# Kernel optimization log

Hardware: AMD Instinct MI355X
Metric: run time of the kernel (lower is better)

The kernel has to match this reference:

```python
import jax, jax.numpy as jnp
import numpy as np

B, N, L = 16, 512, 512          # batch, compound atoms, protein words
DIM = 10                         # compound feature dim
DM, H, DK, DFF = 128, 8, 16, 512 # transformer dims
LG, LO = 3, 3                    # layer_gnn, layer_output
NFP, NW = 10000, 10000           # vocab sizes
NEG = -9e15                      # GAT mask sentinel (matches torch code)


def _layernorm(x, g, b, eps=1e-6):
    # annotated-transformer LayerNorm: unbiased std, eps added to std
    m = jnp.mean(x, -1, keepdims=True)
    s = jnp.std(x, -1, keepdims=True, ddof=1)
    return g * (x - m) / (s + eps) + b


def _pos_encoding(length, d_model):
    pos = np.arange(length)[:, None]
    div = np.exp(np.arange(0, d_model, 2) * (-np.log(10000.0) / d_model))
    pe = np.zeros((length, d_model), np.float32)
    pe[:, 0::2] = np.sin(pos * div)
    pe[:, 1::2] = np.cos(pos * div)
    return jnp.asarray(pe)


def setup_inputs():
    ks = iter(jax.random.split(jax.random.key(0), 64))
    def nrm(shape, scale):
        return jax.random.normal(next(ks), shape, jnp.float32) * scale
    return dict(
        fingerprints=jax.random.randint(next(ks), (B, N), 0, NFP, jnp.int32),
        fp_mask=jnp.ones((B, N), jnp.float32),
        adjacency=jax.random.randint(next(ks), (B, N, N), 0, 2, jnp.int32),
        words=jax.random.randint(next(ks), (B, L), 0, NW, jnp.int32),
        words_mask=jnp.ones((B, L), jnp.float32),
        emb_fp=nrm((NFP, DIM), 0.1),
        emb_word=nrm((NW, DM), 0.1),
        Wg=nrm((LG, DIM, DIM), 0.3), bg=jnp.zeros((LG, DIM), jnp.float32),
        attn_a=nrm((LG, 2 * DIM), 0.3),
        Wq=nrm((DM, DM), 0.09), bq=jnp.zeros((DM,), jnp.float32),
        Wk=nrm((DM, DM), 0.09), bk=jnp.zeros((DM,), jnp.float32),
        Wv=nrm((DM, DM), 0.09), bv=jnp.zeros((DM,), jnp.float32),
        Wo=nrm((DM, DM), 0.09), bo=jnp.zeros((DM,), jnp.float32),
        ln1_g=jnp.ones((DM,), jnp.float32), ln1_b=jnp.zeros((DM,), jnp.float32),
        ln2_g=jnp.ones((DM,), jnp.float32), ln2_b=jnp.zeros((DM,), jnp.float32),
        lnf_g=jnp.ones((DM,), jnp.float32), lnf_b=jnp.zeros((DM,), jnp.float32),
        W1=nrm((DM, DFF), 0.09), b1=jnp.zeros((DFF,), jnp.float32),
        W2=nrm((DFF, DM), 0.045), b2=jnp.zeros((DM,), jnp.float32),
        Wtout=nrm((DM, DIM), 0.09), btout=jnp.zeros((DIM,), jnp.float32),
        Watt=nrm((DIM, DIM), 0.3), batt=jnp.zeros((DIM,), jnp.float32),
        Wout=nrm((LO, 2 * DIM, 2 * DIM), 0.2), bout=jnp.zeros((LO, 2 * DIM), jnp.float32),
        Wint=nrm((2 * DIM, 2), 0.2), bint=jnp.zeros((2,), jnp.float32),
    )


def _forward(fingerprints, fp_mask, adjacency, words, words_mask,
             emb_fp, emb_word, Wg, bg, attn_a,
             Wq, bq, Wk, bk, Wv, bv, Wo, bo,
             ln1_g, ln1_b, ln2_g, ln2_b, lnf_g, lnf_b,
             W1, b1, W2, b2, Wtout, btout,
             Watt, batt, Wout, bout, Wint, bint):
    # ---- GAT over compound graph (dropout disabled = eval/deterministic) ----
    xs = emb_fp[fingerprints]                     # [B,N,DIM]
    mask = fp_mask[:, :, None]                    # [B,N,1]
    adj = adjacency > 0
    for i in range(LG):
        h = jax.nn.relu(xs @ Wg[i] + bg[i]) * mask
        # e[b,i,j] = leaky_relu(a1.h_i + a2.h_j)  == leaky_relu([h_i||h_j] @ a)
        s1 = h @ attn_a[i, :DIM]                  # [B,N]
        s2 = h @ attn_a[i, DIM:]                  # [B,N]
        e = jax.nn.leaky_relu(s1[:, :, None] + s2[:, None, :])  # [B,N,N]
        att = jax.nn.softmax(jnp.where(adj, e, NEG), axis=2)
        xs = xs + att @ h
    compound = jnp.mean(xs * mask, axis=1, keepdims=True)       # [B,1,DIM]

    # ---- transformer encoder, 1 layer, annotated-transformer (pre-norm) ----
    x = emb_word[words] * jnp.sqrt(jnp.float32(DM)) + _pos_encoding(L, DM)
    m4 = words_mask[:, None, None, :] > 0         # [B,1,1,L]
    xn = _layernorm(x, ln1_g, ln1_b)
    heads = lambda t: t.reshape(B, L, H, DK).transpose(0, 2, 1, 3)
    q, k, v = heads(xn @ Wq + bq), heads(xn @ Wk + bk), heads(xn @ Wv + bv)
    scores = jnp.einsum('bhqd,bhkd->bhqk', q, k) / jnp.sqrt(jnp.float32(DK))
    p = jax.nn.softmax(jnp.where(m4, scores, -1e9), axis=-1)
    attn = jnp.einsum('bhqk,bhkd->bhqd', p, v).transpose(0, 2, 1, 3).reshape(B, L, DM)
    x = x + (attn @ Wo + bo)
    xn = _layernorm(x, ln2_g, ln2_b)
    x = x + (jax.nn.relu(xn @ W1 + b1) @ W2 + b2)
    x = _layernorm(x, lnf_g, lnf_b)
    word_vectors = jax.nn.relu(x) @ Wtout + btout  # [B,L,DIM]

    # ---- tanh cross-attention (attention_cnn) ----
    hc = jax.nn.relu(compound @ Watt + batt)       # [B,1,DIM]
    hp = jax.nn.relu(word_vectors @ Watt + batt)   # [B,L,DIM]
    w = jnp.tanh(jnp.einsum('bxd,bld->bxl', hc, hp))  # [B,1,L]
    protein = jnp.mean(w.transpose(0, 2, 1) * hp, axis=1, keepdims=True)  # [B,1,DIM]

    cat = jnp.concatenate([compound, protein], axis=2)  # [B,1,2*DIM]
    for j in range(LO):
        cat = jax.nn.relu(cat @ Wout[j] + bout[j])
    return jnp.squeeze(cat @ Wint + bint, axis=1)        # [B,2]


def reference(fingerprints, fp_mask, adjacency, words, words_mask,
              emb_fp, emb_word, Wg, bg, attn_a,
              Wq, bq, Wk, bk, Wv, bv, Wo, bo,
              ln1_g, ln1_b, ln2_g, ln2_b, lnf_g, lnf_b,
              W1, b1, W2, b2, Wtout, btout,
              Watt, batt, Wout, bout, Wint, bint):
    return _forward(fingerprints, fp_mask, adjacency, words, words_mask,
                    emb_fp, emb_word, Wg, bg, attn_a,
                    Wq, bq, Wk, bk, Wv, bv, Wo, bo,
                    ln1_g, ln1_b, ln2_g, ln2_b, lnf_g, lnf_b,
                    W1, b1, W2, b2, Wtout, btout,
                    Watt, batt, Wout, bout, Wint, bint)
```

## Files before the change

### kernel.cpp

```cpp
#include <hip/hip_runtime.h>
#include <hip/hip_bf16.h>
#include <math.h>

#define B 16
#define N 512
#define L 512
#define DIM 10
#define DM 128
#define H 8
#define DK 16
#define DFF 512
#define LG 3
#define LO 3
#define NEGV -9.0e15f
#define RF 16
#define AQR 64

__device__ __forceinline__ float wave_reduce_sum(float v) {
    #pragma unroll
    for (int o = 32; o > 0; o >>= 1) v += __shfl_down(v, o, 64);
    return v;
}


__global__ void k_embed_fp(const int* __restrict__ fing, const float* __restrict__ emb_fp,
                           float* __restrict__ xs) {
    int idx = blockIdx.x * blockDim.x + threadIdx.x;
    if (idx >= B * N * DIM) return;
    int d = idx % DIM;
    int bn = idx / DIM;
    xs[idx] = emb_fp[fing[bn] * DIM + d];
}

__global__ void k_gnn_h(const float* __restrict__ xs, const float* __restrict__ fp_mask,
                        const float* __restrict__ Wg, const float* __restrict__ bg,
                        const float* __restrict__ aatt,
                        float* __restrict__ h, float* __restrict__ s1, float* __restrict__ s2) {
    int bn = blockIdx.x * blockDim.x + threadIdx.x;
    if (bn >= B * N) return;
    float x[DIM];
    #pragma unroll
    for (int d = 0; d < DIM; d++) x[d] = xs[bn * DIM + d];
    float m = fp_mask[bn];
    float a1 = 0.f, a2 = 0.f;
    #pragma unroll
    for (int j = 0; j < DIM; j++) {
        float acc = bg[j];
        #pragma unroll
        for (int d = 0; d < DIM; d++) acc += x[d] * Wg[d * DIM + j];
        acc = fmaxf(acc, 0.f) * m;
        h[bn * DIM + j] = acc;
        a1 += acc * aatt[j];
        a2 += acc * aatt[DIM + j];
    }
    s1[bn] = a1;
    s2[bn] = a2;
}

__global__ void k_gnn_att(const float* __restrict__ h, const float* __restrict__ s1,
                          const float* __restrict__ s2, const int* __restrict__ adj,
                          float* __restrict__ xs) {
    int b  = blockIdx.x / (N / 16);
    int rg = blockIdx.x % (N / 16);
    int t = threadIdx.x;
    int g  = t >> 4;
    int ll = t & 15;
    int i = rg * 16 + g;

    __shared__ float h_s[N * DIM];
    __shared__ float s2_s[N];

    const float* hb = h + (long)b * N * DIM;
    for (int idx = t; idx < N * DIM; idx += 256) h_s[idx] = hb[idx];
    for (int j = t; j < N; j += 256) s2_s[j] = s2[b * N + j];
    __syncthreads();

    float s1v = s1[b * N + i];
    const int* adjrow = adj + ((long)b * N + i) * N;

    float e[32];
    #pragma unroll
    for (int c = 0; c < 32; c++) {
        int j = c * 16 + ll;
        float xsc = s1v + s2_s[j];
        xsc = xsc > 0.f ? xsc : 0.01f * xsc;
        e[c] = (adjrow[j] > 0) ? xsc : NEGV;
    }
    float m = e[0];
    #pragma unroll
    for (int c = 1; c < 32; c++) m = fmaxf(m, e[c]);
    #pragma unroll
    for (int off = 1; off < 16; off <<= 1) m = fmaxf(m, __shfl_xor(m, off, 64));

    float sum = 0.f;
    float a[DIM];
    #pragma unroll
    for (int d = 0; d < DIM; d++) a[d] = 0.f;
    #pragma unroll
    for (int c = 0; c < 32; c++) {
        float p = expf(e[c] - m);
        sum += p;
        int j = c * 16 + ll;
        #pragma unroll
        for (int d = 0; d < DIM; d++) a[d] += p * h_s[j * DIM + d];
    }
    #pragma unroll
    for (int off = 1; off < 16; off <<= 1) {
        sum += __shfl_xor(sum, off, 64);
        #pragma unroll
        for (int d = 0; d < DIM; d++) a[d] += __shfl_xor(a[d], off, 64);
    }
    if (ll < DIM) {
        float av = a[0];
        if (ll == 1) av = a[1]; else if (ll == 2) av = a[2]; else if (ll == 3) av = a[3];
        else if (ll == 4) av = a[4]; else if (ll == 5) av = a[5]; else if (ll == 6) av = a[6];
        else if (ll == 7) av = a[7]; else if (ll == 8) av = a[8]; else if (ll == 9) av = a[9];
        xs[((long)b * N + i) * DIM + ll] += av / sum;
    }
}

__global__ void k_compound(const float* __restrict__ xs, const float* __restrict__ fp_mask,
                           const float* __restrict__ Watt, const float* __restrict__ batt,
                           float* __restrict__ compound, float* __restrict__ hc) {
    int b = blockIdx.x;
    int t = threadIdx.x;
    int wid = t >> 6, lane = t & 63;
    float lacc[DIM];
    #pragma unroll
    for (int d = 0; d < DIM; d++) lacc[d] = 0.f;
    for (int n = t; n < N; n += 256) {
        float m = fp_mask[b * N + n];
        #pragma unroll
        for (int d = 0; d < DIM; d++) lacc[d] += xs[((long)b * N + n) * DIM + d] * m;
    }
    __shared__ float red[4][DIM];
    __shared__ float comp_s[DIM];
    #pragma unroll
    for (int d = 0; d < DIM; d++) lacc[d] = wave_reduce_sum(lacc[d]);
    if (lane == 0) {
        #pragma unroll
        for (int d = 0; d < DIM; d++) red[wid][d] = lacc[d];
    }
    __syncthreads();
    if (t < DIM) {
        float c = (red[0][t] + red[1][t] + red[2][t] + red[3][t]) / (float)N;
        compound[b * DIM + t] = c;
        comp_s[t] = c;
    }
    __syncthreads();
    if (t < DIM) {
        float acc = batt[t];
        #pragma unroll
        for (int e = 0; e < DIM; e++) acc += comp_s[e] * Watt[e * DIM + t];
        hc[b * DIM + t] = fmaxf(acc, 0.f);
    }
}


__global__ void k_pe(float* __restrict__ pe) {
    int idx = blockIdx.x * blockDim.x + threadIdx.x;
    if (idx >= L * DM) return;
    int d = idx % DM, l = idx / DM;
    int k = d >> 1;
    double div = exp((double)(2 * k) * (-log(10000.0) / (double)DM));
    double ang = (double)l * div;
    pe[idx] = (d & 1) ? (float)cos(ang) : (float)sin(ang);
}

__global__ void k_embed_word(const int* __restrict__ words, const float* __restrict__ emb,
                             const float* __restrict__ pe, float* __restrict__ x) {
    long idx = (long)blockIdx.x * blockDim.x + threadIdx.x;
    if (idx >= (long)B * L * DM) return;
    int d = idx % DM;
    long bl = idx / DM;
    int l = (int)(bl % L);
    x[idx] = emb[(long)words[bl] * DM + d] * sqrtf(128.0f) + pe[l * DM + d];
}

__global__ void k_layernorm(const float* __restrict__ x, const float* __restrict__ g,
                            const float* __restrict__ bb, float* __restrict__ out) {
    int row = blockIdx.x;
    int t = threadIdx.x;
    int wid = t >> 6, lane = t & 63;
    float v = x[(long)row * DM + t];
    float s = wave_reduce_sum(v);
    __shared__ float r2[2], r3[2];
    if (lane == 0) r2[wid] = s;
    __syncthreads();
    float mean = (r2[0] + r2[1]) / (float)DM;
    float dv = v - mean;
    float q = wave_reduce_sum(dv * dv);
    if (lane == 0) r3[wid] = q;
    __syncthreads();
    float sd = sqrtf((r3[0] + r3[1]) / (float)(DM - 1)) + 1e-6f;
    out[(long)row * DM + t] = g[t] * dv / sd + bb[t];
}

__global__ void k_qkv(const float* __restrict__ xn,
                      const float* __restrict__ Wq, const float* __restrict__ bq,
                      const float* __restrict__ Wk, const float* __restrict__ bk,
                      const float* __restrict__ Wv, const float* __restrict__ bv,
                      float* __restrict__ q, float* __restrict__ k, float* __restrict__ v) {
    long row0 = (long)blockIdx.x * RF;
    int t = threadIdx.x;
    __shared__ float xs_s[RF * DM];
    for (int i = t; i < RF * DM; i += 384) xs_s[i] = xn[row0 * DM + i];
    __syncthreads();
    int proj = t / DM;
    int j = t % DM;
    const float* W    = proj == 0 ? Wq : (proj == 1 ? Wk : Wv);
    const float* bias = proj == 0 ? bq : (proj == 1 ? bk : bv);
    float* out        = proj == 0 ? q  : (proj == 1 ? k  : v);
    float acc[RF];
    #pragma unroll
    for (int r = 0; r < RF; r++) acc[r] = bias[j];
    for (int d = 0; d < DM; d++) {
        float w = W[d * DM + j];
        #pragma unroll
        for (int r = 0; r < RF; r++) acc[r] += xs_s[r * DM + d] * w;
    }
    #pragma unroll
    for (int r = 0; r < RF; r++) {
        long row = row0 + r;
        int b = (int)(row / L), l = (int)(row % L);
        out[(((long)b * H + j / DK) * L + l) * DK + (j % DK)] = acc[r];
    }
}

__global__ void k_attn(const float* __restrict__ q, const float* __restrict__ k,
                       const float* __restrict__ v, const float* __restrict__ wmask,
                       float* __restrict__ attnout) {
    int blk = blockIdx.x;
    int qc = blk % (L / AQR);
    int bh = blk / (L / AQR);
    int b = bh / H, hh = bh % H;
    int t = threadIdx.x;
    int sl = t & 3;
    int r = t >> 2;
    int l = qc * AQR + r;

    __shared__ float4 k_s[L * 4];
    __shared__ float wm_s[L];
    const float4* kb4 = (const float4*)(k + (long)bh * L * DK);
    for (int i = t; i < L * 4; i += 256) k_s[i] = kb4[i];
    for (int j = t; j < L; j += 256) wm_s[j] = wmask[b * L + j];
    __syncthreads();

    float4 qr = ((const float4*)(q + ((long)bh * L + l) * DK))[sl];
    qr.x *= 0.25f; qr.y *= 0.25f; qr.z *= 0.25f; qr.w *= 0.25f;

    const float4* vb4 = (const float4*)(v + (long)bh * L * DK);

    float m = -1e30f, ssum = 0.f;
    float4 acc = make_float4(0.f, 0.f, 0.f, 0.f);

    for (int c = 0; c < L / 8; c++) {
        int j0 = c * 8;
        float s8[8];
        #pragma unroll
        for (int jj = 0; jj < 8; jj++) {
            float4 kk = k_s[(j0 + jj) * 4 + sl];
            s8[jj] = qr.x * kk.x + qr.y * kk.y + qr.z * kk.z + qr.w * kk.w;
        }
        #pragma unroll
        for (int jj = 0; jj < 8; jj++) {
            s8[jj] += __shfl_xor(s8[jj], 1, 64);
            s8[jj] += __shfl_xor(s8[jj], 2, 64);
            s8[jj] = (wm_s[j0 + jj] > 0.f) ? s8[jj] : -1e9f;
        }
        float cm = fmaxf(fmaxf(fmaxf(s8[0], s8[1]), fmaxf(s8[2], s8[3])),
                         fmaxf(fmaxf(s8[4], s8[5]), fmaxf(s8[6], s8[7])));
        float mn = fmaxf(m, cm);
        float scale = __expf(m - mn);
        ssum *= scale;
        acc.x *= scale; acc.y *= scale; acc.z *= scale; acc.w *= scale;
        #pragma unroll
        for (int jj = 0; jj < 8; jj++) {
            float p = __expf(s8[jj] - mn);
            ssum += p;
            float4 vv = vb4[(j0 + jj) * 4 + sl];
            acc.x += p * vv.x; acc.y += p * vv.y; acc.z += p * vv.z; acc.w += p * vv.w;
        }
        m = mn;
    }

    float inv = 1.f / ssum;
    float4* outp = (float4*)(attnout + ((long)b * L + l) * DM + hh * DK);
    outp[sl] = make_float4(acc.x * inv, acc.y * inv, acc.z * inv, acc.w * inv);
}

__global__ void k_oproj(const float* __restrict__ attnout, const float* __restrict__ Wo,
                        const float* __restrict__ bo, float* __restrict__ x) {
    long row0 = (long)blockIdx.x * RF;
    int t = threadIdx.x;
    __shared__ float a_s[RF * DM];
    for (int i = t; i < RF * DM; i += 128) a_s[i] = attnout[row0 * DM + i];
    __syncthreads();
    float acc[RF];
    #pragma unroll
    for (int r = 0; r < RF; r++) acc[r] = bo[t];
    for (int d = 0; d < DM; d++) {
        float w = Wo[d * DM + t];
        #pragma unroll
        for (int r = 0; r < RF; r++) acc[r] += a_s[r * DM + d] * w;
    }
    #pragma unroll
    for (int r = 0; r < RF; r++) x[(row0 + r) * DM + t] += acc[r];
}

__global__ void k_ffn(const float* __restrict__ xn, const float* __restrict__ W1,
                      const float* __restrict__ b1, const float* __restrict__ W2,
                      const float* __restrict__ b2, float* __restrict__ x) {
    long row0 = (long)blockIdx.x * RF;
    int t = threadIdx.x;
    __shared__ float xs_s[RF * DM];
    __shared__ float h_s[RF * DFF];
    for (int i = t; i < RF * DM; i += 512) xs_s[i] = xn[row0 * DM + i];
    __syncthreads();
    {
        float acc[RF];
        #pragma unroll
        for (int r = 0; r < RF; r++) acc[r] = b1[t];
        for (int d = 0; d < DM; d++) {
            float w = W1[d * DFF + t];
            #pragma unroll
            for (int r = 0; r < RF; r++) acc[r] += xs_s[r * DM + d] * w;
        }
        #pragma unroll
        for (int r = 0; r < RF; r++) h_s[r * DFF + t] = fmaxf(acc[r], 0.f);
    }
    __syncthreads();
    int col = t & 127, rq = t >> 7;
    float acc2[4];
    #pragma unroll
    for (int rr = 0; rr < 4; rr++) acc2[rr] = b2[col];
    for (int f = 0; f < DFF; f++) {
        float w = W2[f * DM + col];
        #pragma unroll
        for (int rr = 0; rr < 4; rr++) acc2[rr] += h_s[(rq * 4 + rr) * DFF + f] * w;
    }
    #pragma unroll
    for (int rr = 0; rr < 4; rr++) x[(row0 + rq * 4 + rr) * DM + col] += acc2[rr];
}

__global__ void k_lnf_hp(const float* __restrict__ x, const float* __restrict__ g,
                         const float* __restrict__ bb, const float* __restrict__ Wtout,
                         const float* __restrict__ btout, const float* __restrict__ Watt,
                         const float* __restrict__ batt, float* __restrict__ hp) {
    int row = blockIdx.x;
    int t = threadIdx.x;
    int wid = t >> 6, lane = t & 63;
    float v = x[(long)row * DM + t];
    float s = wave_reduce_sum(v);
    __shared__ float r2[2], r3[2];
    if (lane == 0) r2[wid] = s;
    __syncthreads();
    float mean = (r2[0] + r2[1]) / (float)DM;
    float dv = v - mean;
    float qq = wave_reduce_sum(dv * dv);
    if (lane == 0) r3[wid] = qq;
    __syncthreads();
    float sd = sqrtf((r3[0] + r3[1]) / (float)(DM - 1)) + 1e-6f;
    float xnv = g[t] * dv / sd + bb[t];
    __shared__ float rrelu[DM];
    rrelu[t] = fmaxf(xnv, 0.f);
    __syncthreads();
    __shared__ float wv_s[DIM];
    if (t < DIM) {
        float acc = btout[t];
        for (int d = 0; d < DM; d++) acc += rrelu[d] * Wtout[d * DIM + t];
        wv_s[t] = acc;
    }
    __syncthreads();
    if (t < DIM) {
        float acc = batt[t];
        #pragma unroll
        for (int e = 0; e < DIM; e++) acc += wv_s[e] * Watt[e * DIM + t];
        hp[(long)row * DIM + t] = fmaxf(acc, 0.f);
    }
}

__global__ void k_final(const float* __restrict__ hp, const float* __restrict__ hc,
                        const float* __restrict__ compound, const float* __restrict__ Wout,
                        const float* __restrict__ bout, const float* __restrict__ Wint,
                        const float* __restrict__ bint, float* __restrict__ out) {
    int b = blockIdx.x;
    int t = threadIdx.x;
    int wid = t >> 6, lane = t & 63;

    __shared__ float wout_s[LO * 2 * DIM * 2 * DIM];
    __shared__ float bout_s[LO * 2 * DIM];
    __shared__ float wint_s[2 * DIM * 2];
    __shared__ float bint_s[2];
    __shared__ float hc_s[DIM];
    __shared__ float red[4][DIM];
    __shared__ float cat_s[2 * DIM];
    __shared__ float tmp_s[2 * DIM];

    for (int i = t; i < LO * 2 * DIM * 2 * DIM; i += 256) wout_s[i] = Wout[i];
    for (int i = t; i < LO * 2 * DIM; i += 256) bout_s[i] = bout[i];
    for (int i = t; i < 2 * DIM * 2; i += 256) wint_s[i] = Wint[i];
    if (t < 2) bint_s[t] = bint[t];
    if (t < DIM) hc_s[t] = hc[b * DIM + t];
    __syncthreads();

    float lacc[DIM];
    #pragma unroll
    for (int e = 0; e < DIM; e++) lacc[e] = 0.f;
    for (int l = t; l < L; l += 256) {
        const float* hpl = hp + ((long)b * L + l) * DIM;
        float hv[DIM];
        float dot = 0.f;
        #pragma unroll
        for (int e = 0; e < DIM; e++) { hv[e] = hpl[e]; dot += hc_s[e] * hv[e]; }
        float w = tanhf(dot);
        #pragma unroll
        for (int e = 0; e < DIM; e++) lacc[e] += w * hv[e];
    }
    #pragma unroll
    for (int e = 0; e < DIM; e++) lacc[e] = wave_reduce_sum(lacc[e]);
    if (lane == 0) {
        #pragma unroll
        for (int e = 0; e < DIM; e++) red[wid][e] = lacc[e];
    }
    __syncthreads();
    if (t < DIM) {
        cat_s[t] = compound[b * DIM + t];
        cat_s[DIM + t] = (red[0][t] + red[1][t] + red[2][t] + red[3][t]) / (float)L;
    }
    __syncthreads();

    for (int j = 0; j < LO; j++) {
        float acc = 0.f;
        if (t < 2 * DIM) {
            acc = bout_s[j * 2 * DIM + t];
            #pragma unroll
            for (int e = 0; e < 2 * DIM; e++)
                acc += cat_s[e] * wout_s[j * 2 * DIM * 2 * DIM + e * 2 * DIM + t];
            acc = fmaxf(acc, 0.f);
            tmp_s[t] = acc;
        }
        __syncthreads();
        if (t < 2 * DIM) cat_s[t] = tmp_s[t];
        __syncthreads();
    }
    if (t < 2) {
        float o = bint_s[t];
        #pragma unroll
        for (int e = 0; e < 2 * DIM; e++) o += cat_s[e] * wint_s[e * 2 + t];
        out[b * 2 + t] = o;
    }
}

extern "C" void kernel_launch(void* const* d_in, const int* in_sizes, int n_in,
                              void* d_out, int out_size, void* d_ws, size_t ws_size,
                              hipStream_t stream) {
    (void)in_sizes; (void)n_in; (void)out_size; (void)ws_size;
    const int*   fingerprints = (const int*)d_in[0];
    const float* fp_mask      = (const float*)d_in[1];
    const int*   adjacency    = (const int*)d_in[2];
    const int*   words        = (const int*)d_in[3];
    const float* words_mask   = (const float*)d_in[4];
    const float* emb_fp       = (const float*)d_in[5];
    const float* emb_word     = (const float*)d_in[6];
    const float* Wg   = (const float*)d_in[7];
    const float* bg   = (const float*)d_in[8];
    const float* attn_a = (const float*)d_in[9];
    const float* Wq = (const float*)d_in[10];
    const float* bq = (const float*)d_in[11];
    const float* Wk = (const float*)d_in[12];
    const float* bk = (const float*)d_in[13];
    const float* Wv = (const float*)d_in[14];
    const float* bv = (const float*)d_in[15];
    const float* Wo = (const float*)d_in[16];
    const float* bo = (const float*)d_in[17];
    const float* ln1_g = (const float*)d_in[18];
    const float* ln1_b = (const float*)d_in[19];
    const float* ln2_g = (const float*)d_in[20];
    const float* ln2_b = (const float*)d_in[21];
    const float* lnf_g = (const float*)d_in[22];
    const float* lnf_b = (const float*)d_in[23];
    const float* W1 = (const float*)d_in[24];
    const float* b1 = (const float*)d_in[25];
    const float* W2 = (const float*)d_in[26];
    const float* b2 = (const float*)d_in[27];
    const float* Wtout = (const float*)d_in[28];
    const float* btout = (const float*)d_in[29];
    const float* Watt  = (const float*)d_in[30];
    const float* batt  = (const float*)d_in[31];
    const float* Wout  = (const float*)d_in[32];
    const float* bout  = (const float*)d_in[33];
    const float* Wint  = (const float*)d_in[34];
    const float* bint  = (const float*)d_in[35];
    float* out = (float*)d_out;

    float* w = (float*)d_ws;
    float* xs = w;        w += B * N * DIM;
    float* h  = w;        w += B * N * DIM;
    float* s1 = w;        w += B * N;
    float* s2 = w;        w += B * N;
    float* compound = w;  w += B * DIM;
    float* hc = w;        w += B * DIM;
    float* pe = w;        w += L * DM;
    float* x  = w;        w += (long)B * L * DM;
    float* xn = w;        w += (long)B * L * DM;
    float* qb = w;        w += (long)B * H * L * DK;
    float* kb = w;        w += (long)B * H * L * DK;
    float* vb = w;        w += (long)B * H * L * DK;
    float* attnout = w;   w += (long)B * L * DM;
    float* hp = w;        w += (long)B * L * DIM;

    k_embed_fp<<<(B * N * DIM + 255) / 256, 256, 0, stream>>>(fingerprints, emb_fp, xs);
    for (int i = 0; i < LG; i++) {
        k_gnn_h<<<(B * N + 255) / 256, 256, 0, stream>>>(
            xs, fp_mask, Wg + i * DIM * DIM, bg + i * DIM, attn_a + i * 2 * DIM, h, s1, s2);
        k_gnn_att<<<B * (N / 16), 256, 0, stream>>>(h, s1, s2, adjacency, xs);
    }
    k_compound<<<B, 256, 0, stream>>>(xs, fp_mask, Watt, batt, compound, hc);

    k_pe<<<(L * DM + 255) / 256, 256, 0, stream>>>(pe);
    k_embed_word<<<(B * L * DM + 255) / 256, 256, 0, stream>>>(words, emb_word, pe, x);
    k_layernorm<<<B * L, DM, 0, stream>>>(x, ln1_g, ln1_b, xn);
    k_qkv<<<B * L / RF, 3 * DM, 0, stream>>>(xn, Wq, bq, Wk, bk, Wv, bv, qb, kb, vb);
    k_attn<<<B * H * (L / AQR), 256, 0, stream>>>(qb, kb, vb, words_mask, attnout);
    k_oproj<<<B * L / RF, DM, 0, stream>>>(attnout, Wo, bo, x);
    k_layernorm<<<B * L, DM, 0, stream>>>(x, ln2_g, ln2_b, xn);
    k_ffn<<<B * L / RF, DFF, 0, stream>>>(xn, W1, b1, W2, b2, x);
    k_lnf_hp<<<B * L, DM, 0, stream>>>(x, lnf_g, lnf_b, Wtout, btout, Watt, batt, hp);
    k_final<<<B, 256, 0, stream>>>(hp, hc, compound, Wout, bout, Wint, bint, out);
}
```

Before: 277.1 us.

## Restructure attention with split-key threads and double-buffered K/V tiles

Rewrites the attention kernel so each query row is handled by 8 threads that each own a slice of keys, rather than 4 threads splitting the head dimension with shuffle reductions per score. K and V are streamed through double-buffered, swizzled shared-memory tiles of 64 keys, with next-tile global loads issued before compute, and V now comes from LDS instead of global memory. Per-thread online-softmax partials are merged with xor shuffles at the end. The block size doubles to 512 threads with launch bounds of 1, which raises register pressure and adds a barrier per tile.

```diff
diff --git a/kernel.cpp b/kernel.cpp
--- a/kernel.cpp
+++ b/kernel.cpp
@@ -15,11 +15,21 @@
 #define NEGV -9.0e15f
 #define RF 16
 #define AQR 64
+#define KT 64
+#define NT (L / KT)
 
 __device__ __forceinline__ float wave_reduce_sum(float v) {
     #pragma unroll
     for (int o = 32; o > 0; o >>= 1) v += __shfl_down(v, o, 64);
     return v;
+}
+
+__device__ __forceinline__ float dot16(float4 q0, float4 q1, float4 q2, float4 q3,
+                                       float4 k0, float4 k1, float4 k2, float4 k3) {
+    return q0.x*k0.x + q0.y*k0.y + q0.z*k0.z + q0.w*k0.w
+         + q1.x*k1.x + q1.y*k1.y + q1.z*k1.z + q1.w*k1.w
+         + q2.x*k2.x + q2.y*k2.y + q2.z*k2.z + q2.w*k2.w
+         + q3.x*k3.x + q3.y*k3.y + q3.z*k3.z + q3.w*k3.w;
 }
 
 
@@ -227,66 +237,131 @@
     }
 }
 
-__global__ void k_attn(const float* __restrict__ q, const float* __restrict__ k,
-                       const float* __restrict__ v, const float* __restrict__ wmask,
-                       float* __restrict__ attnout) {
+__global__ void __launch_bounds__(512, 1)
+k_attn(const float* __restrict__ q, const float* __restrict__ k,
+       const float* __restrict__ v, const float* __restrict__ wmask,
+       float* __restrict__ attnout) {
     int blk = blockIdx.x;
     int qc = blk % (L / AQR);
     int bh = blk / (L / AQR);
     int b = bh / H, hh = bh % H;
     int t = threadIdx.x;
-    int sl = t & 3;
-    int r = t >> 2;
-    int l = qc * AQR + r;
-
-    __shared__ float4 k_s[L * 4];
-    __shared__ float wm_s[L];
+    int qg = t >> 3;
+    int kg = t & 7;
+    int l = qc * AQR + qg;
+
+    __shared__ float kbuf[2][KT * DK];
+    __shared__ float vbuf[2][KT * DK];
+    __shared__ float madd[2][KT];
+
     const float4* kb4 = (const float4*)(k + (long)bh * L * DK);
-    for (int i = t; i < L * 4; i += 256) k_s[i] = kb4[i];
-    for (int j = t; j < L; j += 256) wm_s[j] = wmask[b * L + j];
-    __syncthreads();
-
-    float4 qr = ((const float4*)(q + ((long)bh * L + l) * DK))[sl];
-    qr.x *= 0.25f; qr.y *= 0.25f; qr.z *= 0.25f; qr.w *= 0.25f;
-
     const float4* vb4 = (const float4*)(v + (long)bh * L * DK);
-
-    float m = -1e30f, ssum = 0.f;
-    float4 acc = make_float4(0.f, 0.f, 0.f, 0.f);
-
-    for (int c = 0; c < L / 8; c++) {
-        int j0 = c * 8;
-        float s8[8];
-        #pragma unroll
-        for (int jj = 0; jj < 8; jj++) {
-            float4 kk = k_s[(j0 + jj) * 4 + sl];
-            s8[jj] = qr.x * kk.x + qr.y * kk.y + qr.z * kk.z + qr.w * kk.w;
+    const float*  wm  = wmask + (long)b * L;
+
+    const float4* qp = (const float4*)(q + ((long)bh * L + l) * DK);
+    float4 q0 = qp[0], q1 = qp[1], q2 = qp[2], q3 = qp[3];
+    q0.x*=0.25f;q0.y*=0.25f;q0.z*=0.25f;q0.w*=0.25f;
+    q1.x*=0.25f;q1.y*=0.25f;q1.z*=0.25f;q1.w*=0.25f;
+    q2.x*=0.25f;q2.y*=0.25f;q2.z*=0.25f;q2.w*=0.25f;
+    q3.x*=0.25f;q3.y*=0.25f;q3.z*=0.25f;q3.w*=0.25f;
+
+    int si = t & 255;
+    int skey = si >> 2, sc = si & 3;
+    int gch = sc ^ ((skey >> 3) & 3);
+    const float4* gsrc = (t < 256) ? kb4 : vb4;
+    long gidx = (long)skey * 4 + gch;
+
+    {
+        float4 r = gsrc[gidx];
+        float* dst = (t < 256) ? &kbuf[0][0] : &vbuf[0][0];
+        ((float4*)dst)[si] = r;
+        if (t < KT) madd[0][t] = (wm[t] > 0.f) ? 0.f : -1e9f;
+    }
+    __syncthreads();
+
+    float m = -1e30f, ss = 0.f;
+    float4 a0 = make_float4(0,0,0,0), a1 = a0, a2 = a0, a3 = a0;
+    int swz = kg & 3;
+
+    int cur = 0;
+    for (int tt = 0; tt < NT; tt++) {
+        float4 pre;
+        float mpre = 1.f;
+        if (tt < NT - 1) {
+            pre = gsrc[(long)(tt + 1) * KT * 4 + gidx];
+            if (t < KT) mpre = wm[(tt + 1) * KT + t];
         }
-        #pragma unroll
-        for (int jj = 0; jj < 8; jj++) {
-            s8[jj] += __shfl_xor(s8[jj], 1, 64);
-            s8[jj] += __shfl_xor(s8[jj], 2, 64);
-            s8[jj] = (wm_s[j0 + jj] > 0.f) ? s8[jj] : -1e9f;
+
+        float s[8];
+        #pragma unroll
+        for (int kk = 0; kk < 8; kk++) {
+            const float4* kp = (const float4*)&kbuf[cur][(kg * 8 + kk) * DK];
+            float4 k0 = kp[0 ^ swz], k1 = kp[1 ^ swz], k2 = kp[2 ^ swz], k3 = kp[3 ^ swz];
+            s[kk] = dot16(q0, q1, q2, q3, k0, k1, k2, k3);
         }
-        float cm = fmaxf(fmaxf(fmaxf(s8[0], s8[1]), fmaxf(s8[2], s8[3])),
-                         fmaxf(fmaxf(s8[4], s8[5]), fmaxf(s8[6], s8[7])));
+        {
+            const float4* mp = (const float4*)&madd[cur][kg * 8];
+            float4 ma = mp[0], mb_ = mp[1];
+            s[0] += ma.x;  s[1] += ma.y;  s[2] += ma.z;  s[3] += ma.w;
+            s[4] += mb_.x; s[5] += mb_.y; s[6] += mb_.z; s[7] += mb_.w;
+        }
+
+        float cm = fmaxf(fmaxf(fmaxf(s[0], s[1]), fmaxf(s[2], s[3])),
+                         fmaxf(fmaxf(s[4], s[5]), fmaxf(s[6], s[7])));
         float mn = fmaxf(m, cm);
         float scale = __expf(m - mn);
-        ssum *= scale;
-        acc.x *= scale; acc.y *= scale; acc.z *= scale; acc.w *= scale;
-        #pragma unroll
-        for (int jj = 0; jj < 8; jj++) {
-            float p = __expf(s8[jj] - mn);
-            ssum += p;
-            float4 vv = vb4[(j0 + jj) * 4 + sl];
-            acc.x += p * vv.x; acc.y += p * vv.y; acc.z += p * vv.z; acc.w += p * vv.w;
+        m = mn;
+        float pls = 0.f;
+        #pragma unroll
+        for (int kk = 0; kk < 8; kk++) { s[kk] = __expf(s[kk] - mn); pls += s[kk]; }
+        ss = ss * scale + pls;
+        a0.x*=scale;a0.y*=scale;a0.z*=scale;a0.w*=scale;
+        a1.x*=scale;a1.y*=scale;a1.z*=scale;a1.w*=scale;
+        a2.x*=scale;a2.y*=scale;a2.z*=scale;a2.w*=scale;
+        a3.x*=scale;a3.y*=scale;a3.z*=scale;a3.w*=scale;
+
+        #pragma unroll
+        for (int kk = 0; kk < 8; kk++) {
+            const float4* vp = (const float4*)&vbuf[cur][(kg * 8 + kk) * DK];
+            float4 v0 = vp[0 ^ swz], v1 = vp[1 ^ swz], v2 = vp[2 ^ swz], v3 = vp[3 ^ swz];
+            float p = s[kk];
+            a0.x += p*v0.x; a0.y += p*v0.y; a0.z += p*v0.z; a0.w += p*v0.w;
+            a1.x += p*v1.x; a1.y += p*v1.y; a1.z += p*v1.z; a1.w += p*v1.w;
+            a2.x += p*v2.x; a2.y += p*v2.y; a2.z += p*v2.z; a2.w += p*v2.w;
+            a3.x += p*v3.x; a3.y += p*v3.y; a3.z += p*v3.z; a3.w += p*v3.w;
         }
+
+        if (tt < NT - 1) {
+            float* dst = (t < 256) ? &kbuf[cur ^ 1][0] : &vbuf[cur ^ 1][0];
+            ((float4*)dst)[si] = pre;
+            if (t < KT) madd[cur ^ 1][t] = (mpre > 0.f) ? 0.f : -1e9f;
+        }
+        __syncthreads();
+        cur ^= 1;
+    }
+
+    #pragma unroll
+    for (int off = 1; off <= 4; off <<= 1) {
+        float m2  = __shfl_xor(m, off, 64);
+        float ss2 = __shfl_xor(ss, off, 64);
+        float mn = fmaxf(m, m2);
+        float ea = __expf(m - mn), eb = __expf(m2 - mn);
+        ss = ss * ea + ss2 * eb;
+        #define MRG(f) { float o_ = __shfl_xor(f, off, 64); f = f * ea + o_ * eb; }
+        MRG(a0.x) MRG(a0.y) MRG(a0.z) MRG(a0.w)
+        MRG(a1.x) MRG(a1.y) MRG(a1.z) MRG(a1.w)
+        MRG(a2.x) MRG(a2.y) MRG(a2.z) MRG(a2.w)
+        MRG(a3.x) MRG(a3.y) MRG(a3.z) MRG(a3.w)
+        #undef MRG
         m = mn;
     }
 
-    float inv = 1.f / ssum;
-    float4* outp = (float4*)(attnout + ((long)b * L + l) * DM + hh * DK);
-    outp[sl] = make_float4(acc.x * inv, acc.y * inv, acc.z * inv, acc.w * inv);
+    if (kg < 4) {
+        float4 ov = (kg == 0) ? a0 : (kg == 1) ? a1 : (kg == 2) ? a2 : a3;
+        float inv = 1.f / ss;
+        float4* outp = (float4*)(attnout + ((long)b * L + l) * DM + hh * DK);
+        outp[kg] = make_float4(ov.x * inv, ov.y * inv, ov.z * inv, ov.w * inv);
+    }
 }
 
 __global__ void k_oproj(const float* __restrict__ attnout, const float* __restrict__ Wo,
@@ -522,7 +597,7 @@
     k_embed_word<<<(B * L * DM + 255) / 256, 256, 0, stream>>>(words, emb_word, pe, x);
     k_layernorm<<<B * L, DM, 0, stream>>>(x, ln1_g, ln1_b, xn);
     k_qkv<<<B * L / RF, 3 * DM, 0, stream>>>(xn, Wq, bq, Wk, bk, Wv, bv, qb, kb, vb);
-    k_attn<<<B * H * (L / AQR), 256, 0, stream>>>(qb, kb, vb, words_mask, attnout);
+    k_attn<<<B * H * (L / AQR), 512, 0, stream>>>(qb, kb, vb, words_mask, attnout);
     k_oproj<<<B * L / RF, DM, 0, stream>>>(attnout, Wo, bo, x);
     k_layernorm<<<B * L, DM, 0, stream>>>(x, ln2_g, ln2_b, xn);
     k_ffn<<<B * L / RF, DFF, 0, stream>>>(xn, W1, b1, W2, b2, x);
```

After: 426.2 us (median of 3 runs). 1.54x slower.
